# Optimization experiments

Hardware: AMD Instinct MI355X
Metric: run time of the kernel (lower is better)

Reference implementation:

```python
import jax, jax.numpy as jnp
import numpy as np

N_NODES = 100_000
N_EDGES = 1_600_000
N_FEAT = 64
HIDDEN = 64
BIOPRINT = 2048
N_GRAPHS = 1024


def setup_inputs() -> dict:
    key = jax.random.key(0)
    ks = jax.random.split(key, 12)
    x = jax.random.normal(ks[0], (N_NODES, N_FEAT), jnp.float32)
    edge_index = jax.random.randint(ks[1], (2, N_EDGES), 0, N_NODES, dtype=jnp.int64)
    batch = jnp.sort(jax.random.randint(ks[2], (N_NODES,), 0, N_GRAPHS, dtype=jnp.int64))
    def lin(k, fan_in, fan_out):
        s = 1.0 / np.sqrt(fan_in)
        return jax.random.uniform(k, (fan_in, fan_out), jnp.float32, -s, s)
    W1 = lin(ks[3], N_FEAT, HIDDEN)
    b1 = jnp.zeros((HIDDEN,), jnp.float32)
    W2 = lin(ks[4], HIDDEN, HIDDEN)
    b2 = jnp.zeros((HIDDEN,), jnp.float32)
    W3 = lin(ks[5], HIDDEN, HIDDEN)
    b3 = jnp.zeros((HIDDEN,), jnp.float32)
    Wd = lin(ks[6], HIDDEN, BIOPRINT)
    bd = jax.random.uniform(ks[7], (BIOPRINT,), jnp.float32, -1.0 / np.sqrt(HIDDEN), 1.0 / np.sqrt(HIDDEN))
    return {"x": x, "edge_index": edge_index, "batch": batch,
            "W1": W1, "b1": b1, "W2": W2, "b2": b2, "W3": W3, "b3": b3,
            "Wd": Wd, "bd": bd}


def reference(x, edge_index, batch, W1, b1, W2, b2, W3, b3, Wd, bd):
    n = x.shape[0]
    src, dst = edge_index[0], edge_index[1]
    # GCN symmetric normalization with self-loops: deg = in-degree + 1
    ones_e = jnp.ones(src.shape[0], x.dtype)
    deg = jax.ops.segment_sum(ones_e, dst, num_segments=n) + 1.0
    dinv = jax.lax.rsqrt(deg)  # deg >= 1 always
    self_norm = (dinv * dinv)[:, None]
    edge_norm = (dinv[src] * dinv[dst])[:, None]

    def gcn_conv(h, W, b):
        hw = h @ W  # [N, out]
        agg = jax.ops.segment_sum(hw[src] * edge_norm, dst, num_segments=n)
        return agg + hw * self_norm + b  # self-loop handled analytically

    h = jax.nn.relu(gcn_conv(x, W1, b1))
    h = jax.nn.relu(gcn_conv(h, W2, b2))
    h = gcn_conv(h, W3, b3)

    # global_mean_pool over graph ids
    cnt = jax.ops.segment_sum(jnp.ones(n, x.dtype), batch, num_segments=N_GRAPHS)
    pooled = jax.ops.segment_sum(h, batch, num_segments=N_GRAPHS) / jnp.maximum(cnt, 1.0)[:, None]

    # dropout(p=0.5) is identity in eval mode
    logits = pooled @ Wd + bd
    probs = jax.nn.softmax(logits, axis=-1)
    return (probs >= 0.5).astype(x.dtype)
```

## Files before the change

kernel.cpp:

```cpp
#include <hip/hip_runtime.h>
#include <hip/hip_fp16.h>
#include <math.h>

#define N_NODES   100000
#define N_EDGES   1600000
#define N_FEAT    64
#define HIDDEN    64
#define BIOPRINT  2048
#define N_GRAPHS  1024

#define SENTINEL  N_NODES
#define ELL_STRIDE 64

#define N_E4 (N_EDGES / 4)
#define DEG_BLOCKS ((N_E4 + 255) / 256)
#define FILL_BLOCKS DEG_BLOCKS
#define MM1_BLOCKS (N_NODES / 32)
#define GS_BLOCKS  5

__device__ __forceinline__ __half2 shx_h2(__half2 v, int m) {
    int x = __shfl_xor(*(int*)&v, m);
    return *(__half2*)&x;
}

__device__ __forceinline__ void stage_w_perm(const float* __restrict__ W, float* sW, int t) {
    const float4* W4 = (const float4*)W;
    for (int i = t; i < 1024; i += 256) {
        float4 w = W4[i];
        int k = i >> 4;
        int c4 = (i & 15) * 4;
        int base = (k >> 2) * 256 + (k & 3);
        sW[base + (c4 + 0) * 4] = w.x;
        sW[base + (c4 + 1) * 4] = w.y;
        sW[base + (c4 + 2) * 4] = w.z;
        sW[base + (c4 + 3) * 4] = w.w;
    }
}

__global__ __launch_bounds__(256) void k_deg(const int* __restrict__ dst,
                                             int* __restrict__ deg,
                                             int* __restrict__ rank) {
    int tid = blockIdx.x * blockDim.x + threadIdx.x;
    if (tid >= N_E4) return;
    int4 d4 = ((const int4*)dst)[tid];
    int4 r4;
    r4.x = atomicAdd(&deg[d4.x], 1);
    r4.y = atomicAdd(&deg[d4.y], 1);
    r4.z = atomicAdd(&deg[d4.z], 1);
    r4.w = atomicAdd(&deg[d4.w], 1);
    ((int4*)rank)[tid] = r4;
}

__global__ __launch_bounds__(256) void k_fillmm(
        const int* __restrict__ src, const int* __restrict__ dst,
        const int* __restrict__ rank, int* __restrict__ colELL,
        const int* __restrict__ deg, float* __restrict__ dinv,
        const float* __restrict__ x, const float* __restrict__ W,
        __half* __restrict__ hw,
        const int* __restrict__ batch, int* __restrict__ gstart) {
    int bid = blockIdx.x, t = threadIdx.x;
    if (bid < FILL_BLOCKS) {
        int tid = bid * 256 + t;
        if (tid < N_E4) {
            int4 d4 = ((const int4*)dst)[tid];
            int4 r4 = ((const int4*)rank)[tid];
            int4 s4 = ((const int4*)src)[tid];
            colELL[d4.x * ELL_STRIDE + (r4.x & 63)] = s4.x;
            colELL[d4.y * ELL_STRIDE + (r4.y & 63)] = s4.y;
            colELL[d4.z * ELL_STRIDE + (r4.z & 63)] = s4.z;
            colELL[d4.w * ELL_STRIDE + (r4.w & 63)] = s4.w;
        }
        return;
    }
    bid -= FILL_BLOCKS;
    if (bid < MM1_BLOCKS) {
        __shared__ float sW[64 * 64];
        __shared__ float sA[32 * 64];
        stage_w_perm(W, sW, t);
        int row0 = bid * 32;
        ((float4*)sA)[t]       = ((const float4*)x)[row0 * 16 + t];
        ((float4*)sA)[t + 256] = ((const float4*)x)[row0 * 16 + t + 256];
        __syncthreads();
        int wave = t >> 6, lane = t & 63;
        const float4* sWp = (const float4*)sW;
        float sum[8] = {0.f, 0.f, 0.f, 0.f, 0.f, 0.f, 0.f, 0.f};
#pragma unroll
        for (int k4 = 0; k4 < 16; ++k4) {
            float4 w4 = sWp[k4 * 64 + lane];
#pragma unroll
            for (int hh = 0; hh < 8; ++hh) {
                float4 a4 = ((const float4*)&sA[(wave * 8 + hh) * 64])[k4];
                sum[hh] = fmaf(a4.x, w4.x, sum[hh]);
                sum[hh] = fmaf(a4.y, w4.y, sum[hh]);
                sum[hh] = fmaf(a4.z, w4.z, sum[hh]);
                sum[hh] = fmaf(a4.w, w4.w, sum[hh]);
            }
        }
#pragma unroll
        for (int hh = 0; hh < 8; ++hh) {
            int row = row0 + wave * 8 + hh;
            float di = rsqrtf((float)deg[row] + 1.0f);
            hw[(size_t)row * 64 + lane] = __float2half_rn(sum[hh] * di);
        }
        if (t < 32) {
            int r2 = row0 + t;
            int dv = deg[r2];
            dinv[r2] = rsqrtf((float)dv + 1.0f);
            if (dv > 64) dv = 64;
            int vp = (dv + 15) & ~15;
            for (int j = dv; j < vp; ++j) colELL[r2 * ELL_STRIDE + j] = SENTINEL;
        }
        return;
    }
    int g = (bid - MM1_BLOCKS) * 256 + t;
    if (g > N_GRAPHS) return;
    if (g == N_GRAPHS) { gstart[g] = N_NODES; return; }
    int lo = 0, hi = N_NODES;
    while (lo < hi) { int mid = (lo + hi) >> 1; if (batch[mid] < g) lo = mid + 1; else hi = mid; }
    gstart[g] = lo;
}

__device__ __forceinline__ void gather2x8(
        const int* __restrict__ col, const uint4* __restrict__ hv,
        int rs, int re, int slot, int sub, float f[8]) {
    __half2 a0 = __float2half2_rn(0.f), a1 = a0, a2 = a0, a3 = a0;
    __half2 c0 = a0, c1 = a0, c2 = a0, c3 = a0;
    for (int e = rs; e < re; e += 16) {
        int s0 = __builtin_nontemporal_load(&col[e + slot]);
        int s1 = __builtin_nontemporal_load(&col[e + 2 + slot]);
        int s2 = __builtin_nontemporal_load(&col[e + 4 + slot]);
        int s3 = __builtin_nontemporal_load(&col[e + 6 + slot]);
        int s4 = __builtin_nontemporal_load(&col[e + 8 + slot]);
        int s5 = __builtin_nontemporal_load(&col[e + 10 + slot]);
        int s6 = __builtin_nontemporal_load(&col[e + 12 + slot]);
        int s7 = __builtin_nontemporal_load(&col[e + 14 + slot]);
        uint4 u0 = hv[(size_t)s0 * 8 + sub];
        uint4 u1 = hv[(size_t)s1 * 8 + sub];
        uint4 u2 = hv[(size_t)s2 * 8 + sub];
        uint4 u3 = hv[(size_t)s3 * 8 + sub];
        uint4 u4 = hv[(size_t)s4 * 8 + sub];
        uint4 u5 = hv[(size_t)s5 * 8 + sub];
        uint4 u6 = hv[(size_t)s6 * 8 + sub];
        uint4 u7 = hv[(size_t)s7 * 8 + sub];
        a0 = __hadd2(a0, *(__half2*)&u0.x); a1 = __hadd2(a1, *(__half2*)&u0.y);
        a2 = __hadd2(a2, *(__half2*)&u0.z); a3 = __hadd2(a3, *(__half2*)&u0.w);
        c0 = __hadd2(c0, *(__half2*)&u1.x); c1 = __hadd2(c1, *(__half2*)&u1.y);
        c2 = __hadd2(c2, *(__half2*)&u1.z); c3 = __hadd2(c3, *(__half2*)&u1.w);
        a0 = __hadd2(a0, *(__half2*)&u2.x); a1 = __hadd2(a1, *(__half2*)&u2.y);
        a2 = __hadd2(a2, *(__half2*)&u2.z); a3 = __hadd2(a3, *(__half2*)&u2.w);
        c0 = __hadd2(c0, *(__half2*)&u3.x); c1 = __hadd2(c1, *(__half2*)&u3.y);
        c2 = __hadd2(c2, *(__half2*)&u3.z); c3 = __hadd2(c3, *(__half2*)&u3.w);
        a0 = __hadd2(a0, *(__half2*)&u4.x); a1 = __hadd2(a1, *(__half2*)&u4.y);
        a2 = __hadd2(a2, *(__half2*)&u4.z); a3 = __hadd2(a3, *(__half2*)&u4.w);
        c0 = __hadd2(c0, *(__half2*)&u5.x); c1 = __hadd2(c1, *(__half2*)&u5.y);
        c2 = __hadd2(c2, *(__half2*)&u5.z); c3 = __hadd2(c3, *(__half2*)&u5.w);
        a0 = __hadd2(a0, *(__half2*)&u6.x); a1 = __hadd2(a1, *(__half2*)&u6.y);
        a2 = __hadd2(a2, *(__half2*)&u6.z); a3 = __hadd2(a3, *(__half2*)&u6.w);
        c0 = __hadd2(c0, *(__half2*)&u7.x); c1 = __hadd2(c1, *(__half2*)&u7.y);
        c2 = __hadd2(c2, *(__half2*)&u7.z); c3 = __hadd2(c3, *(__half2*)&u7.w);
    }
    a0 = __hadd2(a0, c0); a1 = __hadd2(a1, c1);
    a2 = __hadd2(a2, c2); a3 = __hadd2(a3, c3);
    a0 = __hadd2(a0, shx_h2(a0, 8));
    a1 = __hadd2(a1, shx_h2(a1, 8));
    a2 = __hadd2(a2, shx_h2(a2, 8));
    a3 = __hadd2(a3, shx_h2(a3, 8));
    float2 f0 = __half22float2(a0), f1 = __half22float2(a1);
    float2 f2 = __half22float2(a2), f3 = __half22float2(a3);
    f[0] = f0.x; f[1] = f0.y; f[2] = f1.x; f[3] = f1.y;
    f[4] = f2.x; f[5] = f2.y; f[6] = f3.x; f[7] = f3.y;
}

__global__ __launch_bounds__(256) void k_gmm(
        const int* __restrict__ deg, const int* __restrict__ col,
        const float* __restrict__ dinv, const float* __restrict__ b,
        const __half* __restrict__ hw_in, const float* __restrict__ W,
        __half* __restrict__ hw_out) {
    __shared__ float sW[64 * 64];
    __shared__ float sA[16 * 64];
    int t = threadIdx.x;
    stage_w_perm(W, sW, t);
    __syncthreads();

    int wave = t >> 6, lane = t & 63;
    int quarter = lane >> 4, slot = (lane >> 3) & 1, sub = lane & 7;
    int i0 = blockIdx.x * 16 + wave * 4;
    int i = i0 + quarter;
    float di = dinv[i];
    int dv = deg[i]; if (dv > 64) dv = 64;
    int rs = i * ELL_STRIDE;
    int re = rs + ((dv + 15) & ~15);
    const uint4* hv = (const uint4*)hw_in;

    float f[8];
    gather2x8(col, hv, rs, re, slot, sub, f);

    uint4 us = hv[(size_t)i * 8 + sub];
    float2 s0 = __half22float2(*(__half2*)&us.x);
    float2 s1 = __half22float2(*(__half2*)&us.y);
    float2 s2 = __half22float2(*(__half2*)&us.z);
    float2 s3 = __half22float2(*(__half2*)&us.w);
    float sf[8] = {s0.x, s0.y, s1.x, s1.y, s2.x, s2.y, s3.x, s3.y};
    float4 ba = ((const float4*)b)[sub * 2];
    float4 bb = ((const float4*)b)[sub * 2 + 1];
    float bf[8] = {ba.x, ba.y, ba.z, ba.w, bb.x, bb.y, bb.z, bb.w};
    if (slot == 0) {
        float r[8];
#pragma unroll
        for (int k = 0; k < 8; ++k) r[k] = fmaxf(fmaf(di, f[k] + sf[k], bf[k]), 0.f);
        *(float4*)&sA[(wave * 4 + quarter) * 64 + sub * 8]     = make_float4(r[0], r[1], r[2], r[3]);
        *(float4*)&sA[(wave * 4 + quarter) * 64 + sub * 8 + 4] = make_float4(r[4], r[5], r[6], r[7]);
    }

    const float4* sWp = (const float4*)sW;
    float sum[4] = {0.f, 0.f, 0.f, 0.f};
#pragma unroll
    for (int k4 = 0; k4 < 16; ++k4) {
        float4 w4 = sWp[k4 * 64 + lane];
#pragma unroll
        for (int hh = 0; hh < 4; ++hh) {
            float4 a4 = ((const float4*)&sA[(wave * 4 + hh) * 64])[k4];
            sum[hh] = fmaf(a4.x, w4.x, sum[hh]);
            sum[hh] = fmaf(a4.y, w4.y, sum[hh]);
            sum[hh] = fmaf(a4.z, w4.z, sum[hh]);
            sum[hh] = fmaf(a4.w, w4.w, sum[hh]);
        }
    }
#pragma unroll
    for (int hh = 0; hh < 4; ++hh)
        hw_out[(size_t)(i0 + hh) * 64 + lane] = __float2half_rn(sum[hh] * dinv[i0 + hh]);
}

__global__ __launch_bounds__(256) void k_gather3(
        const int* __restrict__ deg, const int* __restrict__ col,
        const float* __restrict__ dinv, const float* __restrict__ b,
        const __half* __restrict__ hw_in, __half* __restrict__ conv) {
    int t = threadIdx.x;
    int wave = t >> 6, lane = t & 63;
    int quarter = lane >> 4, slot = (lane >> 3) & 1, sub = lane & 7;
    int i = blockIdx.x * 16 + wave * 4 + quarter;
    float di = dinv[i];
    int dv = deg[i]; if (dv > 64) dv = 64;
    int rs = i * ELL_STRIDE;
    int re = rs + ((dv + 15) & ~15);
    const uint4* hv = (const uint4*)hw_in;

    float f[8];
    gather2x8(col, hv, rs, re, slot, sub, f);

    if (slot == 0) {
        uint4 us = hv[(size_t)i * 8 + sub];
        float2 s0 = __half22float2(*(__half2*)&us.x);
        float2 s1 = __half22float2(*(__half2*)&us.y);
        float2 s2 = __half22float2(*(__half2*)&us.z);
        float2 s3 = __half22float2(*(__half2*)&us.w);
        float sf[8] = {s0.x, s0.y, s1.x, s1.y, s2.x, s2.y, s3.x, s3.y};
        float4 ba = ((const float4*)b)[sub * 2];
        float4 bb = ((const float4*)b)[sub * 2 + 1];
        float bf[8] = {ba.x, ba.y, ba.z, ba.w, bb.x, bb.y, bb.z, bb.w};
        uint4 o;
        __half2* oh = (__half2*)&o;
#pragma unroll
        for (int c = 0; c < 4; ++c) {
            float r0 = fmaf(di, f[2 * c] + sf[2 * c], bf[2 * c]);
            float r1 = fmaf(di, f[2 * c + 1] + sf[2 * c + 1], bf[2 * c + 1]);
            oh[c] = __halves2half2(__float2half_rn(r0), __float2half_rn(r1));
        }
        ((uint4*)conv)[(size_t)i * 8 + sub] = o;
    }
}

__global__ __launch_bounds__(256) void k_dense(
        const __half* __restrict__ conv, const int* __restrict__ gstart,
        const float* __restrict__ Wd, const float* __restrict__ bd,
        float* __restrict__ out) {
    __shared__ float sred[4][64];
    __shared__ float sp[64];
    __shared__ float rmax[4];
    __shared__ float rsum[4];
    int t = threadIdx.x;
    int wave = t >> 6, lane = t & 63;
    int g = blockIdx.x;
    int n0 = gstart[g], n1 = gstart[g + 1];

    int fp = lane & 31;
    int par = lane >> 5;
    const __half2* conv2 = (const __half2*)conv;
    float2 acc2 = make_float2(0.f, 0.f);
    for (int i = n0 + wave * 2 + par; i < n1; i += 8) {
        float2 f = __half22float2(conv2[(size_t)i * 32 + fp]);
        acc2.x += f.x; acc2.y += f.y;
    }
    acc2.x += __shfl_xor(acc2.x, 32);
    acc2.y += __shfl_xor(acc2.y, 32);
    if (lane < 32) { sred[wave][2 * fp] = acc2.x; sred[wave][2 * fp + 1] = acc2.y; }
    __syncthreads();
    if (t < 64) {
        int n = n1 - n0;
        float s = sred[0][t] + sred[1][t] + sred[2][t] + sred[3][t];
        sp[t] = (n > 0) ? s / (float)n : 0.f;
    }
    __syncthreads();

    float acc[8];
#pragma unroll
    for (int r = 0; r < 8; ++r) acc[r] = bd[r * 256 + t];
    for (int k = 0; k < 64; ++k) {
        float h = sp[k];
#pragma unroll
        for (int r = 0; r < 8; ++r)
            acc[r] = fmaf(h, Wd[k * BIOPRINT + r * 256 + t], acc[r]);
    }

    float m = acc[0];
#pragma unroll
    for (int r = 1; r < 8; ++r) m = fmaxf(m, acc[r]);
#pragma unroll
    for (int off = 32; off > 0; off >>= 1) m = fmaxf(m, __shfl_xor(m, off));
    if (lane == 0) rmax[wave] = m;
    __syncthreads();
    m = fmaxf(fmaxf(rmax[0], rmax[1]), fmaxf(rmax[2], rmax[3]));

    float s = 0.f;
#pragma unroll
    for (int r = 0; r < 8; ++r) { acc[r] = expf(acc[r] - m); s += acc[r]; }
#pragma unroll
    for (int off = 32; off > 0; off >>= 1) s += __shfl_xor(s, off);
    if (lane == 0) rsum[wave] = s;
    __syncthreads();
    s = rsum[0] + rsum[1] + rsum[2] + rsum[3];

#pragma unroll
    for (int r = 0; r < 8; ++r) {
        float p = acc[r] / s;
        out[(size_t)g * BIOPRINT + r * 256 + t] = (p >= 0.5f) ? 1.0f : 0.0f;
    }
}


extern "C" void kernel_launch(void* const* d_in, const int* in_sizes, int n_in,
                              void* d_out, int out_size, void* d_ws, size_t ws_size,
                              hipStream_t stream) {
    const float* x     = (const float*)d_in[0];
    const int*   ei    = (const int*)d_in[1];
    const int*   batch = (const int*)d_in[2];
    const float* W1 = (const float*)d_in[3];
    const float* b1 = (const float*)d_in[4];
    const float* W2 = (const float*)d_in[5];
    const float* b2 = (const float*)d_in[6];
    const float* W3 = (const float*)d_in[7];
    const float* b3 = (const float*)d_in[8];
    const float* Wd = (const float*)d_in[9];
    const float* bd = (const float*)d_in[10];
    float* out = (float*)d_out;

    const int* src = ei;
    const int* dst = ei + N_EDGES;

    char* ws = (char*)d_ws;
    size_t off = 0;
    auto alloc = [&](size_t bytes) {
        void* p = ws + off;
        off += (bytes + 255) & ~(size_t)255;
        return p;
    };
    int*    deg    = (int*)alloc(N_NODES * sizeof(int));
    float*  dinv   = (float*)alloc(N_NODES * sizeof(float));
    int*    rank   = (int*)alloc((size_t)N_EDGES * sizeof(int));
    int*    gstart = (int*)alloc((N_GRAPHS + 1) * sizeof(int));
    int*    colELL = (int*)alloc((size_t)N_NODES * ELL_STRIDE * sizeof(int));
    __half* bufA   = (__half*)alloc((size_t)(N_NODES + 1) * HIDDEN * sizeof(__half));
    __half* bufB   = (__half*)alloc((size_t)(N_NODES + 1) * HIDDEN * sizeof(__half));
    __half* conv   = (__half*)alloc((size_t)N_NODES * HIDDEN * sizeof(__half));

    hipMemsetAsync(deg, 0, N_NODES * sizeof(int), stream);
    hipMemsetAsync(bufA + (size_t)N_NODES * HIDDEN, 0, HIDDEN * sizeof(__half), stream);
    hipMemsetAsync(bufB + (size_t)N_NODES * HIDDEN, 0, HIDDEN * sizeof(__half), stream);

    k_deg<<<DEG_BLOCKS, 256, 0, stream>>>(dst, deg, rank);
    k_fillmm<<<FILL_BLOCKS + MM1_BLOCKS + GS_BLOCKS, 256, 0, stream>>>(
        src, dst, rank, colELL, deg, dinv, x, W1, bufA, batch, gstart);

    const int g16_grid = N_NODES / 16;
    k_gmm<<<g16_grid, 256, 0, stream>>>(deg, colELL, dinv, b1, bufA, W2, bufB);
    k_gmm<<<g16_grid, 256, 0, stream>>>(deg, colELL, dinv, b2, bufB, W3, bufA);
    k_gather3<<<g16_grid, 256, 0, stream>>>(deg, colELL, dinv, b3, bufA, conv);
    k_dense<<<N_GRAPHS, 256, 0, stream>>>(conv, gstart, Wd, bd, out);
}
```

Before: 338.4 us.

## Replace global atomic degree counting with chunked LDS histograms and prefix offsets

Global atomicAdd degree counting is replaced by a k_count kernel. Each block builds a shared-memory histogram for one node slice (1/8 of nodes) over one edge chunk, recording local ranks. A k_prep kernel then scans the per-chunk counts to get degrees, dinv and per-chunk offsets, and the fill kernel adds these offsets to the local ranks. The aim is to remove contended global atomics, but each edge chunk is now read 8 times and a 49×N counts array is written and scanned, adding a kernel launch and extra traffic.

```diff
diff --git a/kernel.cpp b/kernel.cpp
--- a/kernel.cpp
+++ b/kernel.cpp
@@ -13,10 +13,17 @@
 #define ELL_STRIDE 64
 
 #define N_E4 (N_EDGES / 4)
-#define DEG_BLOCKS ((N_E4 + 255) / 256)
-#define FILL_BLOCKS DEG_BLOCKS
+#define FILL_BLOCKS ((N_E4 + 255) / 256)
 #define MM1_BLOCKS (N_NODES / 32)
 #define GS_BLOCKS  5
+
+#define XCD_SLICE 12500
+#define CHUNK_SHIFT 15
+#define CH4 (1 << (CHUNK_SHIFT - 2))
+#define NC 49
+#define SLOT_P 56
+#define CNT_BLOCKS (8 * SLOT_P)
+#define PREP_BLOCKS ((N_NODES + 255) / 256)
 
 __device__ __forceinline__ __half2 shx_h2(__half2 v, int m) {
     int x = __shfl_xor(*(int*)&v, m);
@@ -37,87 +44,117 @@
     }
 }
 
-__global__ __launch_bounds__(256) void k_deg(const int* __restrict__ dst,
-                                             int* __restrict__ deg,
-                                             int* __restrict__ rank) {
-    int tid = blockIdx.x * blockDim.x + threadIdx.x;
-    if (tid >= N_E4) return;
-    int4 d4 = ((const int4*)dst)[tid];
-    int4 r4;
-    r4.x = atomicAdd(&deg[d4.x], 1);
-    r4.y = atomicAdd(&deg[d4.y], 1);
-    r4.z = atomicAdd(&deg[d4.z], 1);
-    r4.w = atomicAdd(&deg[d4.w], 1);
-    ((int4*)rank)[tid] = r4;
-}
-
-__global__ __launch_bounds__(256) void k_fillmm(
-        const int* __restrict__ src, const int* __restrict__ dst,
-        const int* __restrict__ rank, int* __restrict__ colELL,
-        const int* __restrict__ deg, float* __restrict__ dinv,
-        const float* __restrict__ x, const float* __restrict__ W,
-        __half* __restrict__ hw,
+__global__ __launch_bounds__(256) void k_count(
+        const int* __restrict__ dst, int* __restrict__ counts,
+        int* __restrict__ rankl) {
+    int p = blockIdx.x / SLOT_P;
+    int c = blockIdx.x % SLOT_P;
+    if (c >= NC) return;
+    __shared__ int hist[XCD_SLICE];
+    int t = threadIdx.x;
+    for (int i = t; i < XCD_SLICE; i += 256) hist[i] = 0;
+    __syncthreads();
+    int lo = p * XCD_SLICE, hi = lo + XCD_SLICE;
+    int base4 = c * CH4;
+    int end4 = base4 + CH4; if (end4 > N_E4) end4 = N_E4;
+    const int4* dst4 = (const int4*)dst;
+    for (int i4 = base4 + t; i4 < end4; i4 += 256) {
+        int4 d4 = dst4[i4];
+        int e = i4 * 4;
+        if (d4.x >= lo && d4.x < hi) rankl[e + 0] = atomicAdd(&hist[d4.x - lo], 1);
+        if (d4.y >= lo && d4.y < hi) rankl[e + 1] = atomicAdd(&hist[d4.y - lo], 1);
+        if (d4.z >= lo && d4.z < hi) rankl[e + 2] = atomicAdd(&hist[d4.z - lo], 1);
+        if (d4.w >= lo && d4.w < hi) rankl[e + 3] = atomicAdd(&hist[d4.w - lo], 1);
+    }
+    __syncthreads();
+    int* crow = counts + (size_t)c * N_NODES + lo;
+    for (int i = t; i < XCD_SLICE; i += 256) crow[i] = hist[i];
+}
+
+__global__ __launch_bounds__(256) void k_prep(
+        int* __restrict__ counts, int* __restrict__ deg, float* __restrict__ dinv,
         const int* __restrict__ batch, int* __restrict__ gstart) {
     int bid = blockIdx.x, t = threadIdx.x;
-    if (bid < FILL_BLOCKS) {
-        int tid = bid * 256 + t;
-        if (tid < N_E4) {
-            int4 d4 = ((const int4*)dst)[tid];
-            int4 r4 = ((const int4*)rank)[tid];
-            int4 s4 = ((const int4*)src)[tid];
-            colELL[d4.x * ELL_STRIDE + (r4.x & 63)] = s4.x;
-            colELL[d4.y * ELL_STRIDE + (r4.y & 63)] = s4.y;
-            colELL[d4.z * ELL_STRIDE + (r4.z & 63)] = s4.z;
-            colELL[d4.w * ELL_STRIDE + (r4.w & 63)] = s4.w;
+    if (bid < PREP_BLOCKS) {
+        int n = bid * 256 + t;
+        if (n >= N_NODES) return;
+        int s = 0;
+#pragma unroll
+        for (int c = 0; c < NC; ++c) {
+            size_t idx = (size_t)c * N_NODES + n;
+            int v = counts[idx];
+            counts[idx] = s;
+            s += v;
         }
+        deg[n] = s;
+        dinv[n] = rsqrtf((float)s + 1.0f);
         return;
     }
-    bid -= FILL_BLOCKS;
-    if (bid < MM1_BLOCKS) {
-        __shared__ float sW[64 * 64];
-        __shared__ float sA[32 * 64];
-        stage_w_perm(W, sW, t);
-        int row0 = bid * 32;
-        ((float4*)sA)[t]       = ((const float4*)x)[row0 * 16 + t];
-        ((float4*)sA)[t + 256] = ((const float4*)x)[row0 * 16 + t + 256];
-        __syncthreads();
-        int wave = t >> 6, lane = t & 63;
-        const float4* sWp = (const float4*)sW;
-        float sum[8] = {0.f, 0.f, 0.f, 0.f, 0.f, 0.f, 0.f, 0.f};
-#pragma unroll
-        for (int k4 = 0; k4 < 16; ++k4) {
-            float4 w4 = sWp[k4 * 64 + lane];
-#pragma unroll
-            for (int hh = 0; hh < 8; ++hh) {
-                float4 a4 = ((const float4*)&sA[(wave * 8 + hh) * 64])[k4];
-                sum[hh] = fmaf(a4.x, w4.x, sum[hh]);
-                sum[hh] = fmaf(a4.y, w4.y, sum[hh]);
-                sum[hh] = fmaf(a4.z, w4.z, sum[hh]);
-                sum[hh] = fmaf(a4.w, w4.w, sum[hh]);
-            }
-        }
-#pragma unroll
-        for (int hh = 0; hh < 8; ++hh) {
-            int row = row0 + wave * 8 + hh;
-            float di = rsqrtf((float)deg[row] + 1.0f);
-            hw[(size_t)row * 64 + lane] = __float2half_rn(sum[hh] * di);
-        }
-        if (t < 32) {
-            int r2 = row0 + t;
-            int dv = deg[r2];
-            dinv[r2] = rsqrtf((float)dv + 1.0f);
-            if (dv > 64) dv = 64;
-            int vp = (dv + 15) & ~15;
-            for (int j = dv; j < vp; ++j) colELL[r2 * ELL_STRIDE + j] = SENTINEL;
-        }
-        return;
-    }
-    int g = (bid - MM1_BLOCKS) * 256 + t;
+    int g = (bid - PREP_BLOCKS) * 256 + t;
     if (g > N_GRAPHS) return;
     if (g == N_GRAPHS) { gstart[g] = N_NODES; return; }
     int lo = 0, hi = N_NODES;
     while (lo < hi) { int mid = (lo + hi) >> 1; if (batch[mid] < g) lo = mid + 1; else hi = mid; }
     gstart[g] = lo;
+}
+
+__global__ __launch_bounds__(256) void k_fillmm(
+        const int* __restrict__ src, const int* __restrict__ dst,
+        const int* __restrict__ rankl, const int* __restrict__ counts,
+        int* __restrict__ colELL,
+        const int* __restrict__ deg, const float* __restrict__ dinv,
+        const float* __restrict__ x, const float* __restrict__ W,
+        __half* __restrict__ hw) {
+    int bid = blockIdx.x, t = threadIdx.x;
+    if (bid < FILL_BLOCKS) {
+        int tid = bid * 256 + t;
+        if (tid < N_E4) {
+            int e = tid * 4;
+            const int* pref = counts + (size_t)(e >> CHUNK_SHIFT) * N_NODES;
+            int4 d4 = ((const int4*)dst)[tid];
+            int4 r4 = ((const int4*)rankl)[tid];
+            int4 s4 = ((const int4*)src)[tid];
+            int px = pref[d4.x] + r4.x; colELL[d4.x * ELL_STRIDE + (px & 63)] = s4.x;
+            int py = pref[d4.y] + r4.y; colELL[d4.y * ELL_STRIDE + (py & 63)] = s4.y;
+            int pz = pref[d4.z] + r4.z; colELL[d4.z * ELL_STRIDE + (pz & 63)] = s4.z;
+            int pw = pref[d4.w] + r4.w; colELL[d4.w * ELL_STRIDE + (pw & 63)] = s4.w;
+        }
+        return;
+    }
+    bid -= FILL_BLOCKS;
+    __shared__ float sW[64 * 64];
+    __shared__ float sA[32 * 64];
+    stage_w_perm(W, sW, t);
+    int row0 = bid * 32;
+    ((float4*)sA)[t]       = ((const float4*)x)[row0 * 16 + t];
+    ((float4*)sA)[t + 256] = ((const float4*)x)[row0 * 16 + t + 256];
+    __syncthreads();
+    int wave = t >> 6, lane = t & 63;
+    const float4* sWp = (const float4*)sW;
+    float sum[8] = {0.f, 0.f, 0.f, 0.f, 0.f, 0.f, 0.f, 0.f};
+#pragma unroll
+    for (int k4 = 0; k4 < 16; ++k4) {
+        float4 w4 = sWp[k4 * 64 + lane];
+#pragma unroll
+        for (int hh = 0; hh < 8; ++hh) {
+            float4 a4 = ((const float4*)&sA[(wave * 8 + hh) * 64])[k4];
+            sum[hh] = fmaf(a4.x, w4.x, sum[hh]);
+            sum[hh] = fmaf(a4.y, w4.y, sum[hh]);
+            sum[hh] = fmaf(a4.z, w4.z, sum[hh]);
+            sum[hh] = fmaf(a4.w, w4.w, sum[hh]);
+        }
+    }
+#pragma unroll
+    for (int hh = 0; hh < 8; ++hh) {
+        int row = row0 + wave * 8 + hh;
+        hw[(size_t)row * 64 + lane] = __float2half_rn(sum[hh] * dinv[row]);
+    }
+    if (t < 32) {
+        int r2 = row0 + t;
+        int dv = deg[r2]; if (dv > 64) dv = 64;
+        int vp = (dv + 15) & ~15;
+        for (int j = dv; j < vp; ++j) colELL[r2 * ELL_STRIDE + j] = SENTINEL;
+    }
 }
 
 __device__ __forceinline__ void gather2x8(
@@ -368,18 +405,19 @@
     float*  dinv   = (float*)alloc(N_NODES * sizeof(float));
     int*    rank   = (int*)alloc((size_t)N_EDGES * sizeof(int));
     int*    gstart = (int*)alloc((N_GRAPHS + 1) * sizeof(int));
+    int*    counts = (int*)alloc((size_t)NC * N_NODES * sizeof(int));
     int*    colELL = (int*)alloc((size_t)N_NODES * ELL_STRIDE * sizeof(int));
     __half* bufA   = (__half*)alloc((size_t)(N_NODES + 1) * HIDDEN * sizeof(__half));
     __half* bufB   = (__half*)alloc((size_t)(N_NODES + 1) * HIDDEN * sizeof(__half));
     __half* conv   = (__half*)alloc((size_t)N_NODES * HIDDEN * sizeof(__half));
 
-    hipMemsetAsync(deg, 0, N_NODES * sizeof(int), stream);
     hipMemsetAsync(bufA + (size_t)N_NODES * HIDDEN, 0, HIDDEN * sizeof(__half), stream);
     hipMemsetAsync(bufB + (size_t)N_NODES * HIDDEN, 0, HIDDEN * sizeof(__half), stream);
 
-    k_deg<<<DEG_BLOCKS, 256, 0, stream>>>(dst, deg, rank);
-    k_fillmm<<<FILL_BLOCKS + MM1_BLOCKS + GS_BLOCKS, 256, 0, stream>>>(
-        src, dst, rank, colELL, deg, dinv, x, W1, bufA, batch, gstart);
+    k_count<<<CNT_BLOCKS, 256, 0, stream>>>(dst, counts, rank);
+    k_prep<<<PREP_BLOCKS + GS_BLOCKS, 256, 0, stream>>>(counts, deg, dinv, batch, gstart);
+    k_fillmm<<<FILL_BLOCKS + MM1_BLOCKS, 256, 0, stream>>>(
+        src, dst, rank, counts, colELL, deg, dinv, x, W1, bufA);
 
     const int g16_grid = N_NODES / 16;
     k_gmm<<<g16_grid, 256, 0, stream>>>(deg, colELL, dinv, b1, bufA, W2, bufB);
```

Measured after the change: 316.4 us. -6.5%, faster.
